# Performance work log

Measured on AMD Instinct MI355X. Metric: run time of the kernel, lower is better.

Reference implementation:

```python
import jax, jax.numpy as jnp
import numpy as np

LAYERS, BLOCKS = 10, 4
RES_CH, DIL_CH, SKIP_CH, CLASSES = 32, 32, 512, 256
K = 2                      # kernel_size
OUTPUT_LENGTH = 4096
N_LAYERS = LAYERS * BLOCKS
DILATIONS = [2 ** i for _ in range(BLOCKS) for i in range(LAYERS)]
BATCH, SEQ = 8, 8192       # SEQ divisible by max dilation 512; SEQ - 4092 >= OUTPUT_LENGTH


def conv1d(x, w, dilation=1):
    # x: (N, C_in, L), w: (C_out, C_in, K); causal valid dilated conv
    return jax.lax.conv_general_dilated(
        x, w, window_strides=(1,), padding='VALID',
        rhs_dilation=(dilation,), dimension_numbers=('NCH', 'OIH', 'NCH'))


def setup_inputs() -> dict:
    key = jax.random.key(0)
    ks = jax.random.split(key, 8)
    s = 0.1
    return {
        'x': jax.random.normal(ks[0], (BATCH, 1, SEQ), jnp.float32),
        'start_w': jax.random.normal(ks[1], (RES_CH, 1, 1), jnp.float32) * s,
        'filter_w': jax.random.normal(ks[2], (N_LAYERS, DIL_CH, RES_CH, K), jnp.float32) * s,
        'gate_w': jax.random.normal(ks[3], (N_LAYERS, DIL_CH, RES_CH, K), jnp.float32) * s,
        'res_w': jax.random.normal(ks[4], (N_LAYERS, RES_CH, DIL_CH, 1), jnp.float32) * s,
        'skip_w': jax.random.normal(ks[5], (N_LAYERS, SKIP_CH, DIL_CH, 1), jnp.float32) * s,
        'end_w': jax.random.normal(ks[6], (CLASSES, SKIP_CH, 1), jnp.float32) * s,
        'end_b': jax.random.normal(ks[7], (CLASSES,), jnp.float32) * s,
    }


def reference(x, start_w, filter_w, gate_w, res_w, skip_w, end_w, end_b):
    h = conv1d(x, start_w)                       # (N, RES_CH, SEQ)
    skip = None
    for i in range(N_LAYERS):
        d = DILATIONS[i]
        f = jnp.tanh(conv1d(h, filter_w[i], d))   # (N, DIL_CH, L - d*(K-1))
        g = jax.nn.sigmoid(conv1d(h, gate_w[i], d))
        z = f * g
        s = conv1d(z, skip_w[i])                  # (N, SKIP_CH, L')
        skip = s if skip is None else skip[:, :, -s.shape[2]:] + s
        h = conv1d(z, res_w[i]) + h[:, :, d * (K - 1):]
    out = conv1d(jax.nn.relu(skip), end_w) + end_b[None, :, None]
    out = out[:, :, -OUTPUT_LENGTH:]              # (N, CLASSES, OUTPUT_LENGTH)
    n, c, l = out.shape
    return out.transpose(0, 2, 1).reshape(n * l, c)
```

## Files before the change

kernel.cpp:

```cpp
#include <hip/hip_runtime.h>
#include <hip/hip_bf16.h>


#define BATCH   8
#define SEQ     8192
#define RES_CH  32
#define DIL_CH  32
#define SKIP_CH 512
#define CLASSES 256
#define NLAYERS 40
#define OUTLEN  4096
#define PSTART  (SEQ - OUTLEN)
#define QTOT    (NLAYERS * DIL_CH)

typedef __attribute__((ext_vector_type(8))) short bf16x8;
typedef __attribute__((ext_vector_type(4))) short short4_t;
typedef __attribute__((ext_vector_type(4))) float f32x4;

__device__ __forceinline__ short f2bf(float x) {
    __bf16 b = (__bf16)x;
    return __builtin_bit_cast(short, b);
}
__device__ __forceinline__ float bf2f(short s) {
    return __uint_as_float(((unsigned)(unsigned short)s) << 16);
}
__device__ __forceinline__ float zact(float f, float g) {
    float a = __expf(fminf(-2.0f * f, 80.0f));
    float b = __expf(fminf(-g, 80.0f));
    return (1.0f - a) * __builtin_amdgcn_rcpf((1.0f + a) * (1.0f + b));
}
__device__ __forceinline__ int tswz(int row, int cb) {
    return row * 64 + (cb ^ (((row & 3) << 4) | ((row & 4) << 3)));
}

#define GLOAD_LDS16(g, l)                                                    \
    __builtin_amdgcn_global_load_lds(                                        \
        (const __attribute__((address_space(1))) unsigned int*)(g),          \
        (__attribute__((address_space(3))) unsigned int*)(l), 16, 0, 0)

__global__ __launch_bounds__(256) void k_prep(
    const float* __restrict__ x, const float* __restrict__ sw,
    const float* __restrict__ fw, const float* __restrict__ gw,
    const float* __restrict__ rw, const float* __restrict__ wsk,
    const float* __restrict__ ew,
    float* __restrict__ hf, short* __restrict__ hb,
    short* __restrict__ wA, short* __restrict__ wR,
    short* __restrict__ wskB, short* __restrict__ ewB)
{
    const int gt = blockIdx.x * 256 + threadIdx.x;
    const int gn = gridDim.x * 256;
    for (int idx = gt; idx < BATCH * SEQ; idx += gn) {
        float v = x[idx];
        float* hp = hf + (size_t)idx * RES_CH;
        short* bp = hb + (size_t)idx * RES_CH;
#pragma unroll
        for (int c = 0; c < RES_CH; ++c) {
            float t = v * sw[c];
            hp[c] = t;
            bp[c] = f2bf(t);
        }
    }
    for (int idx = gt; idx < NLAYERS * 64 * 64; idx += gn) {
        int k = idx & 63, rho = (idx >> 6) & 63, i = idx >> 12;
        int tap = k >> 5, c = k & 31;
        int fgsel = rho >> 5, rr = rho & 31;
        int fp = rr >> 4, gg = (rr >> 2) & 3, e = rr & 3;
        int o = gg * 8 + fp * 4 + e;
        float v = fgsel ? gw[((i * 32 + o) * 32 + c) * 2 + tap]
                        : fw[((i * 32 + o) * 32 + c) * 2 + tap];
        wA[idx] = f2bf(v);
    }
    for (int idx = gt; idx < NLAYERS * 1024; idx += gn)
        wR[idx] = f2bf(rw[idx]);
    for (int idx = gt; idx < SKIP_CH * QTOT; idx += gn) {
        int s = idx / QTOT, q = idx - s * QTOT;
        int i = q >> 5, o = q & 31;
        wskB[idx] = f2bf(wsk[((size_t)i * SKIP_CH + s) * 32 + o]);
    }
    for (int idx = gt; idx < CLASSES * SKIP_CH; idx += gn)
        ewB[idx] = f2bf(ew[idx]);
}

template<bool OWNED>
__device__ __forceinline__ void chunk_body(
    int cp0, bool bglob, bool last, int d, int tog,
    const short* __restrict__ hbb, const float* __restrict__ hfb,
    float* __restrict__ hfo, short* __restrict__ hbo,
    short* __restrict__ zbb, int liq,
    const char* trd, char* tw,
    const bf16x8 (&av)[4][2], const bf16x8 (&avr)[2],
    f32x4 (*carryc)[2][2],
    int r, int g14)
{
    int pl[2]; bool pv[2];
#pragma unroll
    for (int fj = 0; fj < 2; ++fj) {
        int p = cp0 + fj * 16 + r;
        pv[fj] = p < SEQ;
        pl[fj] = pv[fj] ? p : SEQ - 1;
    }

    bf16x8 bv[2][2];
    if (bglob) {
#pragma unroll
        for (int fj = 0; fj < 2; ++fj) {
            bv[fj][0] = *(const bf16x8*)(hbb + (pl[fj] - d) * 32 + g14 * 8);
            bv[fj][1] = *(const bf16x8*)(hbb + pl[fj] * 32 + g14 * 8);
        }
    } else {
#pragma unroll
        for (int fj = 0; fj < 2; ++fj) {
            int tr = pl[fj] - tog;
            bv[fj][0] = *(const bf16x8*)(trd + tswz(tr - d, g14 * 16));
            bv[fj][1] = *(const bf16x8*)(trd + tswz(tr, g14 * 16));
        }
    }

    const f32x4 zero4 = {0.f, 0.f, 0.f, 0.f};
    f32x4 acc[4][2];
#pragma unroll
    for (int fi = 0; fi < 4; ++fi)
#pragma unroll
        for (int fj = 0; fj < 2; ++fj) acc[fi][fj] = zero4;
#pragma unroll
    for (int kt = 0; kt < 2; ++kt)
#pragma unroll
        for (int fi = 0; fi < 4; ++fi)
#pragma unroll
            for (int fj = 0; fj < 2; ++fj)
                acc[fi][fj] = __builtin_amdgcn_mfma_f32_16x16x32_bf16(
                    av[fi][kt], bv[fj][kt], acc[fi][fj], 0, 0, 0);

    bf16x8 zv8[2];
#pragma unroll
    for (int fj = 0; fj < 2; ++fj)
#pragma unroll
        for (int fp = 0; fp < 2; ++fp)
#pragma unroll
            for (int e = 0; e < 4; ++e)
                zv8[fj][fp * 4 + e] =
                    f2bf(zact(acc[fp][fj][e], acc[fp + 2][fj][e]));

    if constexpr (OWNED) {
#pragma unroll
        for (int fj = 0; fj < 2; ++fj)
            if (pv[fj] && pl[fj] >= PSTART) {
                short* zp = zbb + (size_t)(pl[fj] - PSTART) * QTOT + liq;
                *(bf16x8*)(zp + g14 * 8) = zv8[fj];
            }
    }

    f32x4 racc[2][2];
    if constexpr (OWNED) {
        if (bglob) {
#pragma unroll
            for (int fi = 0; fi < 2; ++fi)
#pragma unroll
                for (int fj = 0; fj < 2; ++fj)
                    racc[fi][fj] = *(const f32x4*)(hfb + pl[fj] * 32 + fi * 16 + g14 * 4);
        } else {
#pragma unroll
            for (int fi = 0; fi < 2; ++fi)
#pragma unroll
                for (int fj = 0; fj < 2; ++fj)
                    racc[fi][fj] = (*carryc)[fi][fj];
        }
    } else {
#pragma unroll
        for (int fj = 0; fj < 2; ++fj)
#pragma unroll
            for (int fi = 0; fi < 2; ++fi) {
                short4_t hv;
                if (bglob)
                    hv = *(const short4_t*)(hbb + pl[fj] * 32 + fi * 16 + g14 * 4);
                else
                    hv = *(const short4_t*)(trd + tswz(pl[fj] - tog, fi * 32 + g14 * 8));
                f32x4 cv;
#pragma unroll
                for (int e = 0; e < 4; ++e) cv[e] = bf2f(hv[e]);
                racc[fi][fj] = cv;
            }
    }

#pragma unroll
    for (int fi = 0; fi < 2; ++fi)
#pragma unroll
        for (int fj = 0; fj < 2; ++fj)
            racc[fi][fj] = __builtin_amdgcn_mfma_f32_16x16x32_bf16(
                avr[fi], zv8[fj], racc[fi][fj], 0, 0, 0);

    if constexpr (OWNED) {
#pragma unroll
        for (int fi = 0; fi < 2; ++fi)
#pragma unroll
            for (int fj = 0; fj < 2; ++fj)
                (*carryc)[fi][fj] = racc[fi][fj];
    }

    if (!last) {
#pragma unroll
        for (int fj = 0; fj < 2; ++fj)
            if (pv[fj]) {
                int tr = pl[fj] - tog;
#pragma unroll
                for (int fi = 0; fi < 2; ++fi) {
                    short4_t sv;
#pragma unroll
                    for (int e = 0; e < 4; ++e) sv[e] = f2bf(racc[fi][fj][e]);
                    *(short4_t*)(tw + tswz(tr, fi * 32 + g14 * 8)) = sv;
                }
            }
    } else {
        if constexpr (OWNED) {
#pragma unroll
            for (int fj = 0; fj < 2; ++fj)
                if (pv[fj]) {
#pragma unroll
                    for (int fi = 0; fi < 2; ++fi) {
                        *(f32x4*)(hfo + pl[fj] * 32 + fi * 16 + g14 * 4) = racc[fi][fj];
                        short4_t sv;
#pragma unroll
                        for (int e = 0; e < 4; ++e) sv[e] = f2bf(racc[fi][fj][e]);
                        *(short4_t*)(hbo + pl[fj] * 32 + fi * 16 + g14 * 4) = sv;
                    }
                }
        }
    }
}

template<int LC, int S, int TH, int NTB>
__global__ __launch_bounds__(512, 2) void k_fused8(
    const float* __restrict__ hfin, const short* __restrict__ hbin,
    float* __restrict__ hfout, short* __restrict__ hbout,
    const short* __restrict__ wAg, const short* __restrict__ wRg,
    short* __restrict__ Z, int li0, int pminIn, int hsum, int segbase)
{
    constexpr int TROWS = TH + S;
    __shared__ short tile[NTB][TROWS][32];

    const int lane = threadIdx.x & 63;
    const int w    = threadIdx.x >> 6;
    const int r = lane & 15, g14 = lane >> 4;
    const int b = blockIdx.y;
    const int seg0 = segbase + blockIdx.x * S;
    const int tog  = seg0 - TH;

    const float* hfb = hfin + (size_t)b * SEQ * RES_CH;
    const short* hbb = hbin + (size_t)b * SEQ * RES_CH;
    float* hfo = hfout + (size_t)b * SEQ * RES_CH;
    short* hbo = hbout + (size_t)b * SEQ * RES_CH;
    short* zbb = Z + (size_t)b * OUTLEN * QTOT;

    f32x4 carry[2][2];
    int Ht = hsum, pmt = pminIn;

#pragma unroll 1
    for (int t = 0; t < LC; ++t) {
        const int d = 1 << ((li0 + t) % 10);
        Ht -= d; pmt += d;
        const bool bglob = (t == 0);
        const bool last  = (t == LC - 1);
        const short* wAl = wAg + (li0 + t) * 4096;
        const short* wRl = wRg + (li0 + t) * 1024;
        const int liq = (li0 + t) * DIL_CH;
        char* tw = (char*)&tile[t & (NTB - 1)][0][0];
        const char* trd = (const char*)&tile[(t + NTB - 1) & (NTB - 1)][0][0];

        bf16x8 av[4][2];
#pragma unroll
        for (int fi = 0; fi < 4; ++fi)
#pragma unroll
            for (int kt = 0; kt < 2; ++kt)
                av[fi][kt] = *(const bf16x8*)(wAl + (fi * 16 + r) * 64 + kt * 32 + g14 * 8);
        bf16x8 avr[2];
#pragma unroll
        for (int fi = 0; fi < 2; ++fi)
            avr[fi] = *(const bf16x8*)(wRl + (fi * 16 + r) * 32 + g14 * 8);

        {
            const int cp0 = seg0 + w * 32;
            chunk_body<true>(cp0, bglob, last, d, tog, hbb, hfb, hfo, hbo,
                             zbb, liq, trd, tw, av, avr, &carry, r, g14);
        }
        int lo = seg0 - Ht; if (lo < pmt) lo = pmt;
        const int nh = (seg0 - lo + 31) >> 5;
#pragma unroll 1
        for (int hc = w; hc < nh; hc += 8) {
            const int cp0 = seg0 - (hc + 1) * 32;
            chunk_body<false>(cp0, bglob, last, d, tog, hbb, hfb, hfo, hbo,
                              zbb, liq, trd, tw, av, avr, nullptr, r, g14);
        }
        __syncthreads();
    }
}

__global__ __launch_bounds__(256) void k_skip_m97(
    const short* __restrict__ Z, const short* __restrict__ wskB,
    short* __restrict__ skipb)
{
    __shared__ short At[2][128 * 32];
    __shared__ short Bt[2][128 * 32];

    const int bid = blockIdx.x;
    const int b    = bid & 7;
    const int rest = bid >> 3;
    const int sb   = rest & 3;
    const int pb   = rest >> 2;
    const int s0   = sb * 128;
    const int p0   = pb * 128;

    const int lane = threadIdx.x & 63;
    const int w    = threadIdx.x >> 6;
    const int r = lane & 15, g14 = lane >> 4;
    const int soff = (w >> 1) * 64;
    const int poff = (w & 1) * 64;

    const short* Ab = wskB + (size_t)s0 * QTOT;
    const short* Bb = Z + ((size_t)b * OUTLEN + p0) * QTOT;

    const int rb = w * 32;
    const int l4 = lane >> 2;
    const int c4 = lane & 3;
    const int csw = c4 ^ ((l4 >> 1) & 3);
    const int rsw = (g14 ^ ((r >> 1) & 3)) * 8;

#define SK_STAGE(bf, kt)                                                      \
    {                                                                         \
        _Pragma("unroll") for (int j = 0; j < 2; ++j) {                       \
            const short* ga = Ab + (size_t)(rb + j * 16 + l4) * QTOT          \
                                 + (kt) * 32 + csw * 8;                       \
            GLOAD_LDS16(ga, &At[bf][(rb + j * 16) * 32]);                     \
            const short* gb = Bb + (size_t)(rb + j * 16 + l4) * QTOT          \
                                 + (kt) * 32 + csw * 8;                       \
            GLOAD_LDS16(gb, &Bt[bf][(rb + j * 16) * 32]);                     \
        }                                                                     \
    }

    f32x4 acc[4][4];
    const f32x4 zero4 = {0.f, 0.f, 0.f, 0.f};
#pragma unroll
    for (int fi = 0; fi < 4; ++fi)
#pragma unroll
        for (int fj = 0; fj < 4; ++fj) acc[fi][fj] = zero4;

    SK_STAGE(0, 0)
    __syncthreads();

    int cur = 0;
#pragma unroll 1
    for (int kt = 0; kt < QTOT / 32; ++kt) {
        if (kt + 1 < QTOT / 32) SK_STAGE(cur ^ 1, kt + 1)

        bf16x8 av[4], bv[4];
#pragma unroll
        for (int fi = 0; fi < 4; ++fi)
            av[fi] = *(const bf16x8*)&At[cur][(soff + fi * 16 + r) * 32 + rsw];
#pragma unroll
        for (int fj = 0; fj < 4; ++fj)
            bv[fj] = *(const bf16x8*)&Bt[cur][(poff + fj * 16 + r) * 32 + rsw];

#pragma unroll
        for (int fi = 0; fi < 4; ++fi)
#pragma unroll
            for (int fj = 0; fj < 4; ++fj)
                acc[fi][fj] = __builtin_amdgcn_mfma_f32_16x16x32_bf16(
                    av[fi], bv[fj], acc[fi][fj], 0, 0, 0);

        __syncthreads();
        cur ^= 1;
    }

    short* skb = skipb + (size_t)b * OUTLEN * SKIP_CH;
#pragma unroll
    for (int fj = 0; fj < 4; ++fj) {
        int p = p0 + poff + fj * 16 + r;
#pragma unroll
        for (int fi = 0; fi < 4; ++fi) {
            int s = s0 + soff + fi * 16 + g14 * 4;
            short4_t v;
#pragma unroll
            for (int e = 0; e < 4; ++e) v[e] = f2bf(fmaxf(acc[fi][fj][e], 0.f));
            *(short4_t*)(skb + (size_t)p * SKIP_CH + s) = v;
        }
    }
}

__global__ __launch_bounds__(256) void k_end_m97(
    const short* __restrict__ skipB, const short* __restrict__ ewB,
    const float* __restrict__ eb, float* __restrict__ out)
{
    __shared__ short At[2][128 * 32];
    __shared__ short Bt[2][128 * 32];

    const int bid = blockIdx.x;
    const int b    = bid & 7;
    const int rest = bid >> 3;
    const int cb   = rest & 1;
    const int pb   = rest >> 1;
    const int c0   = cb * 128;
    const int p0   = pb * 128;

    const int lane = threadIdx.x & 63;
    const int w    = threadIdx.x >> 6;
    const int r = lane & 15, g14 = lane >> 4;
    const int soff = (w >> 1) * 64;
    const int poff = (w & 1) * 64;

    const short* Ab = ewB + (size_t)c0 * SKIP_CH;
    const short* Bb = skipB + ((size_t)b * OUTLEN + p0) * SKIP_CH;

    const int rb = w * 32;
    const int l4 = lane >> 2;
    const int c4 = lane & 3;
    const int csw = c4 ^ ((l4 >> 1) & 3);
    const int rsw = (g14 ^ ((r >> 1) & 3)) * 8;

#define EK_STAGE(bf, kt)                                                      \
    {                                                                         \
        _Pragma("unroll") for (int j = 0; j < 2; ++j) {                       \
            const short* ga = Ab + (size_t)(rb + j * 16 + l4) * SKIP_CH       \
                                 + (kt) * 32 + csw * 8;                       \
            GLOAD_LDS16(ga, &At[bf][(rb + j * 16) * 32]);                     \
            const short* gb = Bb + (size_t)(rb + j * 16 + l4) * SKIP_CH       \
                                 + (kt) * 32 + csw * 8;                       \
            GLOAD_LDS16(gb, &Bt[bf][(rb + j * 16) * 32]);                     \
        }                                                                     \
    }

    f32x4 acc[4][4];
    const f32x4 zero4 = {0.f, 0.f, 0.f, 0.f};
#pragma unroll
    for (int fi = 0; fi < 4; ++fi)
#pragma unroll
        for (int fj = 0; fj < 4; ++fj) acc[fi][fj] = zero4;

    EK_STAGE(0, 0)
    __syncthreads();

    int cur = 0;
#pragma unroll 1
    for (int kt = 0; kt < SKIP_CH / 32; ++kt) {
        if (kt + 1 < SKIP_CH / 32) EK_STAGE(cur ^ 1, kt + 1)

        bf16x8 av[4], bv[4];
#pragma unroll
        for (int fi = 0; fi < 4; ++fi)
            av[fi] = *(const bf16x8*)&At[cur][(soff + fi * 16 + r) * 32 + rsw];
#pragma unroll
        for (int fj = 0; fj < 4; ++fj)
            bv[fj] = *(const bf16x8*)&Bt[cur][(poff + fj * 16 + r) * 32 + rsw];

#pragma unroll
        for (int fi = 0; fi < 4; ++fi)
#pragma unroll
            for (int fj = 0; fj < 4; ++fj)
                acc[fi][fj] = __builtin_amdgcn_mfma_f32_16x16x32_bf16(
                    av[fi], bv[fj], acc[fi][fj], 0, 0, 0);

        __syncthreads();
        cur ^= 1;
    }

#pragma unroll
    for (int fj = 0; fj < 4; ++fj) {
        int p = p0 + poff + fj * 16 + r;
#pragma unroll
        for (int fi = 0; fi < 4; ++fi) {
            int cls = c0 + soff + fi * 16 + g14 * 4;
            f32x4 bias = *(const f32x4*)(eb + cls);
            f32x4 v;
#pragma unroll
            for (int e = 0; e < 4; ++e) v[e] = acc[fi][fj][e] + bias[e];
            *(f32x4*)(out + ((size_t)b * OUTLEN + p) * CLASSES + cls) = v;
        }
    }
}

extern "C" void kernel_launch(void* const* d_in, const int* in_sizes, int n_in,
                              void* d_out, int out_size, void* d_ws, size_t ws_size,
                              hipStream_t stream) {
    const float* x   = (const float*)d_in[0];
    const float* sw  = (const float*)d_in[1];
    const float* fw  = (const float*)d_in[2];
    const float* gw  = (const float*)d_in[3];
    const float* rw  = (const float*)d_in[4];
    const float* wsk = (const float*)d_in[5];
    const float* ew  = (const float*)d_in[6];
    const float* eb  = (const float*)d_in[7];
    float* out = (float*)d_out;

    const size_t HN = (size_t)BATCH * SEQ * RES_CH;
    float* hf0 = (float*)d_ws;
    float* hf1 = hf0 + HN;
    short* hb0 = (short*)(hf1 + HN);
    short* hb1 = hb0 + HN;
    short* Z     = hb1 + HN;
    short* skipb = Z + (size_t)BATCH * OUTLEN * QTOT;
    short* wA    = skipb + (size_t)BATCH * OUTLEN * SKIP_CH;
    short* wR    = wA + NLAYERS * 64 * 64;
    short* wskB  = wR + NLAYERS * 32 * 32;
    short* ewB   = wskB + (size_t)SKIP_CH * QTOT;

    k_prep<<<dim3(1024), 256, 0, stream>>>(x, sw, fw, gw, rw, wsk, ew,
                                           hf0, hb0, wA, wR, wskB, ewB);

    float* hf[2] = {hf0, hf1};
    short* hb[2] = {hb0, hb1};
    int cur = 0, pmin = 0;
    for (int dec = 0; dec < 4; ++dec) {
        int li0 = dec * 10;
        int segbase = pmin + 255;
        int nseg = (SEQ - segbase + 255) / 256;
        k_fused8<8, 256, 288, 2><<<dim3(nseg, BATCH), 512, 0, stream>>>(
            hf[cur], hb[cur], hf[cur ^ 1], hb[cur ^ 1], wA, wR, Z,
            li0, pmin, 255, segbase);
        cur ^= 1; pmin = segbase;
        segbase = pmin + 768;
        nseg = (SEQ - segbase + 255) / 256;
        k_fused8<2, 256, 512, 1><<<dim3(nseg, BATCH), 512, 0, stream>>>(
            hf[cur], hb[cur], hf[cur ^ 1], hb[cur ^ 1], wA, wR, Z,
            li0 + 8, pmin, 768, segbase);
        cur ^= 1; pmin = segbase;
    }

    k_skip_m97<<<dim3(1024), 256, 0, stream>>>(Z, wskB, skipb);
    k_end_m97<<<dim3(512), 256, 0, stream>>>(skipb, ewB, eb, out);
}
```

Before: 327.3 us.

## Rewrite skip GEMM as 256x256-tile, 8-wave, 8-phase pipelined kernel

Replaces the 128x128-tile skip-projection GEMM with a 256x256 tile computed by 512 threads, K step of 64, and 128KB of double-buffered LDS with XOR swizzling. The main loop is split into eight phases that interleave async global-to-LDS staging with MFMA work, using explicit vmcnt waits, s_barriers and setprio. The aim is more operand reuse per LDS load and better overlap of loads with matrix math. In exchange only 256 blocks launch at one block per CU, so occupancy is lower and the hand-written wait counts have to be exactly right.

```diff
diff --git a/kernel.cpp b/kernel.cpp
--- a/kernel.cpp
+++ b/kernel.cpp
@@ -294,126 +294,130 @@
     }
 }
 
-__global__ __launch_bounds__(256) void k_skip_m97(
+__global__ __launch_bounds__(512, 1) void k_skip_8ph(
     const short* __restrict__ Z, const short* __restrict__ wskB,
     short* __restrict__ skipb)
 {
-    __shared__ short At[2][128 * 32];
-    __shared__ short Bt[2][128 * 32];
+    __shared__ short lds[2][32768];
 
     const int bid = blockIdx.x;
-    const int b    = bid & 7;
-    const int rest = bid >> 3;
-    const int sb   = rest & 3;
-    const int pb   = rest >> 2;
-    const int s0   = sb * 128;
-    const int p0   = pb * 128;
-
-    const int lane = threadIdx.x & 63;
-    const int w    = threadIdx.x >> 6;
-    const int r = lane & 15, g14 = lane >> 4;
-    const int soff = (w >> 1) * 64;
-    const int poff = (w & 1) * 64;
-
-    const short* Ab = wskB + (size_t)s0 * QTOT;
-    const short* Bb = Z + ((size_t)b * OUTLEN + p0) * QTOT;
-
-    const int rb = w * 32;
-    const int l4 = lane >> 2;
-    const int c4 = lane & 3;
-    const int csw = c4 ^ ((l4 >> 1) & 3);
-    const int rsw = (g14 ^ ((r >> 1) & 3)) * 8;
-
-#define SK_STAGE(bf, kt)                                                      \
+    const int b   = bid & 7;
+    const int sb  = (bid >> 3) & 1;
+    const int pb  = bid >> 4;
+    const int s0  = sb * 256;
+    const int p0  = pb * 256;
+
+    const int tid  = threadIdx.x;
+    const int lane = tid & 63;
+    const int w    = tid >> 6;
+    const int wm   = w >> 2;
+    const int wn   = w & 3;
+    const int r = lane & 15, g = lane >> 4;
+
+    const short* Ag = wskB + (size_t)s0 * QTOT;
+    const short* Bg = Z + ((size_t)b * OUTLEN + p0) * QTOT;
+
+    const int srow = tid >> 3;
+    const int sblk = tid & 7;
+
+#define STG(PI, ISA, HH, KT)                                                  \
     {                                                                         \
         _Pragma("unroll") for (int j = 0; j < 2; ++j) {                       \
-            const short* ga = Ab + (size_t)(rb + j * 16 + l4) * QTOT          \
-                                 + (kt) * 32 + csw * 8;                       \
-            GLOAD_LDS16(ga, &At[bf][(rb + j * 16) * 32]);                     \
-            const short* gb = Bb + (size_t)(rb + j * 16 + l4) * QTOT          \
-                                 + (kt) * 32 + csw * 8;                       \
-            GLOAD_LDS16(gb, &Bt[bf][(rb + j * 16) * 32]);                     \
+            int grow = (HH) * 128 + j * 64 + srow;                            \
+            const short* gp = ((ISA) ? Ag : Bg) + (size_t)grow * QTOT         \
+                              + (KT) * 64 + ((sblk ^ (grow & 7)) * 8);        \
+            short* lp = &lds[PI][((ISA) ? 0 : 16384) +                        \
+                                 ((HH) * 128 + j * 64 + w * 8) * 64];         \
+            GLOAD_LDS16(gp, lp);                                              \
         }                                                                     \
     }
 
-    f32x4 acc[4][4];
+#define DS_A(dst, bufi, fi_, kk_)                                             \
+    { int row_ = wm * 128 + (fi_) * 16 + r;                                   \
+      dst = *(const bf16x8*)&lds[bufi][row_ * 64 + ((((kk_) * 4 + g) ^ (row_ & 7)) * 8)]; }
+#define DS_B(dst, bufi, fj_, kk_)                                             \
+    { int row_ = wn * 64 + (fj_) * 16 + r;                                    \
+      dst = *(const bf16x8*)&lds[bufi][16384 + row_ * 64 + ((((kk_) * 4 + g) ^ (row_ & 7)) * 8)]; }
+
+#define FENCE asm volatile("" ::: "memory")
+#define VM4   asm volatile("s_waitcnt vmcnt(4)" ::: "memory")
+
+#define PHASE(BUF, FIB, READB, STAGECODE, VMW)                                \
+    {                                                                         \
+        if (READB) {                                                          \
+            _Pragma("unroll") for (int fj = 0; fj < 4; ++fj)                  \
+                _Pragma("unroll") for (int kk = 0; kk < 2; ++kk)              \
+                    DS_B(bv[fj][kk], BUF, fj, kk);                            \
+        }                                                                     \
+        bf16x8 a0k0, a0k1, a1k0, a1k1;                                        \
+        DS_A(a0k0, BUF, FIB, 0); DS_A(a0k1, BUF, FIB, 1);                     \
+        DS_A(a1k0, BUF, (FIB) + 1, 0); DS_A(a1k1, BUF, (FIB) + 1, 1);         \
+        STAGECODE;                                                            \
+        VMW;                                                                  \
+        FENCE; __builtin_amdgcn_s_barrier(); FENCE;                           \
+        __builtin_amdgcn_s_setprio(1);                                        \
+        _Pragma("unroll") for (int fj = 0; fj < 4; ++fj) {                    \
+            acc[FIB][fj] = __builtin_amdgcn_mfma_f32_16x16x32_bf16(           \
+                a0k0, bv[fj][0], acc[FIB][fj], 0, 0, 0);                      \
+            acc[FIB][fj] = __builtin_amdgcn_mfma_f32_16x16x32_bf16(           \
+                a0k1, bv[fj][1], acc[FIB][fj], 0, 0, 0);                      \
+            acc[(FIB) + 1][fj] = __builtin_amdgcn_mfma_f32_16x16x32_bf16(     \
+                a1k0, bv[fj][0], acc[(FIB) + 1][fj], 0, 0, 0);                \
+            acc[(FIB) + 1][fj] = __builtin_amdgcn_mfma_f32_16x16x32_bf16(     \
+                a1k1, bv[fj][1], acc[(FIB) + 1][fj], 0, 0, 0);                \
+        }                                                                     \
+        __builtin_amdgcn_s_setprio(0);                                        \
+        FENCE; __builtin_amdgcn_s_barrier(); FENCE;                           \
+    }
+
+    f32x4 acc[8][4];
     const f32x4 zero4 = {0.f, 0.f, 0.f, 0.f};
 #pragma unroll
-    for (int fi = 0; fi < 4; ++fi)
+    for (int fi = 0; fi < 8; ++fi)
 #pragma unroll
         for (int fj = 0; fj < 4; ++fj) acc[fi][fj] = zero4;
 
-    SK_STAGE(0, 0)
-    __syncthreads();
-
-    int cur = 0;
+    bf16x8 bv[4][2];
+
+    STG(0, 1, 0, 0) STG(0, 1, 1, 0) STG(0, 0, 0, 0) STG(0, 0, 1, 0)
+    STG(1, 0, 0, 1) STG(1, 0, 1, 1)
+    VM4;
+    FENCE; __builtin_amdgcn_s_barrier(); FENCE;
+
+    const int NIT = QTOT / 128;
 #pragma unroll 1
-    for (int kt = 0; kt < QTOT / 32; ++kt) {
-        if (kt + 1 < QTOT / 32) SK_STAGE(cur ^ 1, kt + 1)
-
-        bf16x8 av[4], bv[4];
-#pragma unroll
-        for (int fi = 0; fi < 4; ++fi)
-            av[fi] = *(const bf16x8*)&At[cur][(soff + fi * 16 + r) * 32 + rsw];
-#pragma unroll
-        for (int fj = 0; fj < 4; ++fj)
-            bv[fj] = *(const bf16x8*)&Bt[cur][(poff + fj * 16 + r) * 32 + rsw];
-
-#pragma unroll
-        for (int fi = 0; fi < 4; ++fi)
-#pragma unroll
-            for (int fj = 0; fj < 4; ++fj)
-                acc[fi][fj] = __builtin_amdgcn_mfma_f32_16x16x32_bf16(
-                    av[fi], bv[fj], acc[fi][fj], 0, 0, 0);
-
-        __syncthreads();
-        cur ^= 1;
+    for (int i = 0; i < NIT; ++i) {
+        const int k1 = 2 * i + 1;
+        const int k2 = 2 * i + 2, k3 = 2 * i + 3;
+        const bool more = (i + 1 < NIT);
+        PHASE(0, 0, 1, STG(1, 1, 0, k1), )
+        PHASE(0, 2, 0, STG(1, 1, 1, k1), )
+        PHASE(0, 4, 0, if (more) STG(0, 0, 0, k2), )
+        PHASE(0, 6, 0, if (more) STG(0, 0, 1, k2), VM4)
+        PHASE(1, 0, 1, if (more) STG(0, 1, 0, k2), )
+        PHASE(1, 2, 0, if (more) STG(0, 1, 1, k2), )
+        PHASE(1, 4, 0, if (more) STG(1, 0, 0, k3), )
+        PHASE(1, 6, 0, if (more) STG(1, 0, 1, k3), VM4)
     }
 
     short* skb = skipb + (size_t)b * OUTLEN * SKIP_CH;
 #pragma unroll
     for (int fj = 0; fj < 4; ++fj) {
-        int p = p0 + poff + fj * 16 + r;
-#pragma unroll
-        for (int fi = 0; fi < 4; ++fi) {
-            int s = s0 + soff + fi * 16 + g14 * 4;
+        int p = p0 + wn * 64 + fj * 16 + r;
+#pragma unroll
+        for (int fi = 0; fi < 8; ++fi) {
+            int s = s0 + wm * 128 + fi * 16 + g * 4;
             short4_t v;
 #pragma unroll
             for (int e = 0; e < 4; ++e) v[e] = f2bf(fmaxf(acc[fi][fj][e], 0.f));
             *(short4_t*)(skb + (size_t)p * SKIP_CH + s) = v;
         }
     }
-}
-
-__global__ __launch_bounds__(256) void k_end_m97(
-    const short* __restrict__ skipB, const short* __restrict__ ewB,
-    const float* __restrict__ eb, float* __restrict__ out)
-{
-    __shared__ short At[2][128 * 32];
-    __shared__ short Bt[2][128 * 32];
-
-    const int bid = blockIdx.x;
-    const int b    = bid & 7;
-    const int rest = bid >> 3;
-    const int cb   = rest & 1;
-    const int pb   = rest >> 1;
-    const int c0   = cb * 128;
-    const int p0   = pb * 128;
-
-    const int lane = threadIdx.x & 63;
-    const int w    = threadIdx.x >> 6;
-    const int r = lane & 15, g14 = lane >> 4;
-    const int soff = (w >> 1) * 64;
-    const int poff = (w & 1) * 64;
-
-    const short* Ab = ewB + (size_t)c0 * SKIP_CH;
-    const short* Bb = skipB + ((size_t)b * OUTLEN + p0) * SKIP_CH;
-
-    const int rb = w * 32;
-    const int l4 = lane >> 2;
-    const int c4 = lane & 3;
-    const int csw = c4 ^ ((l4 >> 1) & 3);
-    const int rsw = (g14 ^ ((r >> 1) & 3)) * 8;
+#undef PHASE
+#undef STG
+#undef DS_A
+#undef DS_B
+}
 
 #define EK_STAGE(bf, kt)                                                      \
     {                                                                         \
@@ -426,6 +430,36 @@
             GLOAD_LDS16(gb, &Bt[bf][(rb + j * 16) * 32]);                     \
         }                                                                     \
     }
+
+__global__ __launch_bounds__(256) void k_end_m97(
+    const short* __restrict__ skipB, const short* __restrict__ ewB,
+    const float* __restrict__ eb, float* __restrict__ out)
+{
+    __shared__ short At[2][128 * 32];
+    __shared__ short Bt[2][128 * 32];
+
+    const int bid = blockIdx.x;
+    const int b    = bid & 7;
+    const int rest = bid >> 3;
+    const int cb   = rest & 1;
+    const int pb   = rest >> 1;
+    const int c0   = cb * 128;
+    const int p0   = pb * 128;
+
+    const int lane = threadIdx.x & 63;
+    const int w    = threadIdx.x >> 6;
+    const int r = lane & 15, g14 = lane >> 4;
+    const int soff = (w >> 1) * 64;
+    const int poff = (w & 1) * 64;
+
+    const short* Ab = ewB + (size_t)c0 * SKIP_CH;
+    const short* Bb = skipB + ((size_t)b * OUTLEN + p0) * SKIP_CH;
+
+    const int rb = w * 32;
+    const int l4 = lane >> 2;
+    const int c4 = lane & 3;
+    const int csw = c4 ^ ((l4 >> 1) & 3);
+    const int rsw = (g14 ^ ((r >> 1) & 3)) * 8;
 
     f32x4 acc[4][4];
     const f32x4 zero4 = {0.f, 0.f, 0.f, 0.f};
@@ -523,6 +557,6 @@
         cur ^= 1; pmin = segbase;
     }
 
-    k_skip_m97<<<dim3(1024), 256, 0, stream>>>(Z, wskB, skipb);
+    k_skip_8ph<<<dim3(256), 512, 0, stream>>>(Z, wskB, skipb);
     k_end_m97<<<dim3(512), 256, 0, stream>>>(skipb, ewB, eb, out);
 }
```

New measurement: 304.0 us. 1.08x faster.
